# Performance work log

Hardware: AMD Instinct MI355X
Metric: run time of the kernel (lower is better)

## Reference

```python
import jax, jax.numpy as jnp
import numpy as np

B, T, A, H = 2048, 512, 32, 16


def setup_inputs() -> dict:
    key = jax.random.key(0)
    ks = jax.random.split(key, 10)
    s = 1.0 / np.sqrt(H)
    inputs = jax.random.normal(ks[0], (B, T, A), dtype=jnp.float32)
    masks = (jax.random.uniform(ks[1], (B, T)) > 0.05).astype(jnp.float32)
    h0 = jnp.zeros((1, B, H), dtype=jnp.float32)
    c0 = jnp.zeros((1, B, H), dtype=jnp.float32)
    # torch nn.LSTM params (gate order i,f,g,o) and linear heads
    w_ih = jax.random.uniform(ks[2], (4 * H, A), minval=-s, maxval=s)
    w_hh = jax.random.uniform(ks[3], (4 * H, H), minval=-s, maxval=s)
    b_ih = jax.random.uniform(ks[4], (4 * H,), minval=-s, maxval=s)
    b_hh = jax.random.uniform(ks[5], (4 * H,), minval=-s, maxval=s)
    w_actor = jax.random.uniform(ks[6], (A, H), minval=-s, maxval=s)
    b_actor = jax.random.uniform(ks[7], (A,), minval=-s, maxval=s)
    w_critic = jax.random.uniform(ks[8], (1, H), minval=-s, maxval=s)
    b_critic = jax.random.uniform(ks[9], (1,), minval=-s, maxval=s)
    return {"inputs": inputs, "masks": masks, "h0": h0, "c0": c0,
            "w_ih": w_ih, "w_hh": w_hh, "b_ih": b_ih, "b_hh": b_hh,
            "w_actor": w_actor, "b_actor": b_actor,
            "w_critic": w_critic, "b_critic": b_critic}


def reference(inputs, masks, h0, c0, w_ih, w_hh, b_ih, b_hh,
              w_actor, b_actor, w_critic, b_critic):
    # masked LSTM scan: state is zeroed where mask==0 before each step
    def step(carry, xm):
        h, c = carry                      # [B,H]
        x, m = xm                         # x:[B,A], m:[B]
        h = h * m[:, None]
        c = c * m[:, None]
        gates = x @ w_ih.T + b_ih + h @ w_hh.T + b_hh   # [B,4H]
        i, f, g, o = jnp.split(gates, 4, axis=-1)
        i = jax.nn.sigmoid(i)
        f = jax.nn.sigmoid(f)
        g = jnp.tanh(g)
        o = jax.nn.sigmoid(o)
        c2 = f * c + i * g
        h2 = o * jnp.tanh(c2)
        return (h2, c2), h2

    xs = (jnp.swapaxes(inputs, 0, 1), masks.T)          # time-major
    (hT, cT), feats = jax.lax.scan(step, (h0[0], c0[0]), xs)
    feats = jnp.swapaxes(feats, 0, 1)                   # [B,T,H]
    actor = feats @ w_actor.T + b_actor                 # [B,T,A]
    critic = feats @ w_critic.T + b_critic              # [B,T,1]
    return actor, critic, hT[None], cT[None]
```

## Files before the change

### kernel.cpp

```cpp
#include <hip/hip_runtime.h>
#include <stdint.h>

#define Bn 2048
#define Tn 512
#define An 32
#define Hn 16

typedef __attribute__((ext_vector_type(8))) short bf16x8;
typedef __attribute__((ext_vector_type(4))) float f32x4;

union FragU { bf16x8 v; uint32_t u[4]; };

static __device__ __forceinline__ uint32_t pack_hi16(float a, float b){
  return (__float_as_uint(b) & 0xFFFF0000u) | (__float_as_uint(a) >> 16);
}
static __device__ __forceinline__ void split8(const float* s, FragU& hi, FragU& lo){
#pragma unroll
  for (int d = 0; d < 4; ++d){
    float a = s[2*d], b = s[2*d+1];
    float ah = __uint_as_float(__float_as_uint(a) & 0xFFFF0000u);
    float bh = __uint_as_float(__float_as_uint(b) & 0xFFFF0000u);
    hi.u[d] = pack_hi16(a, b);
    lo.u[d] = pack_hi16(a - ah, b - bh);
  }
}
static __device__ __forceinline__ uint32_t plo(uint32_t e, uint32_t o){
  return __builtin_amdgcn_perm(o, e, 0x05040100u);
}
static __device__ __forceinline__ uint32_t phi(uint32_t e, uint32_t o){
  return __builtin_amdgcn_perm(o, e, 0x07060302u);
}
static __device__ __forceinline__ f32x4 MF(const FragU& a, const FragU& b, f32x4 c){
  return __builtin_amdgcn_mfma_f32_16x16x32_bf16(a.v, b.v, c, 0, 0, 0);
}
static __device__ __forceinline__ void packH(const float* hs, uint32_t* pk){
#pragma unroll
  for (int r = 0; r < 4; ++r){
    float hh_ = __uint_as_float(__float_as_uint(hs[r]) & 0xFFFF0000u);
    pk[r] = (__float_as_uint(hs[r] - hh_) & 0xFFFF0000u) | (__float_as_uint(hs[r]) >> 16);
  }
}
static __device__ __forceinline__ void buildBH(const uint32_t* pk, int srcA, int srcB,
                                               FragU& BHh, FragU& BHl){
  uint32_t d0 = (uint32_t)__builtin_amdgcn_ds_bpermute(srcA, (int)pk[0]);
  uint32_t d1 = (uint32_t)__builtin_amdgcn_ds_bpermute(srcA, (int)pk[1]);
  uint32_t d2 = (uint32_t)__builtin_amdgcn_ds_bpermute(srcA, (int)pk[2]);
  uint32_t d3 = (uint32_t)__builtin_amdgcn_ds_bpermute(srcA, (int)pk[3]);
  uint32_t d4 = (uint32_t)__builtin_amdgcn_ds_bpermute(srcB, (int)pk[0]);
  uint32_t d5 = (uint32_t)__builtin_amdgcn_ds_bpermute(srcB, (int)pk[1]);
  uint32_t d6 = (uint32_t)__builtin_amdgcn_ds_bpermute(srcB, (int)pk[2]);
  uint32_t d7 = (uint32_t)__builtin_amdgcn_ds_bpermute(srcB, (int)pk[3]);
  BHh.u[0] = plo(d0, d1); BHh.u[1] = plo(d2, d3);
  BHh.u[2] = plo(d4, d5); BHh.u[3] = plo(d6, d7);
  BHl.u[0] = phi(d0, d1); BHl.u[1] = phi(d2, d3);
  BHl.u[2] = phi(d4, d5); BHl.u[3] = phi(d6, d7);
}

__global__ __launch_bounds__(64, 1)
void lstm_fused(const float* __restrict__ xin,
                const float* __restrict__ masks,
                const float* __restrict__ h0,
                const float* __restrict__ c0,
                const float* __restrict__ w_ih,
                const float* __restrict__ w_hh,
                const float* __restrict__ b_ih,
                const float* __restrict__ b_hh,
                const float* __restrict__ w_act,
                const float* __restrict__ b_act,
                const float* __restrict__ w_cr,
                const float* __restrict__ b_cr,
                float* __restrict__ actor,
                float* __restrict__ critic,
                float* __restrict__ hT,
                float* __restrict__ cT)
{
  const int l = threadIdx.x;
  const int q = l >> 4;
  const int n = l & 15;
  const int b0 = blockIdx.x * 16;
  const int colbase = (q & 1) * 8;
  const bool hiQuad = (q < 2);

  const float KS = -1.44269504088896f;
  const float KG =  2.88539008177793f;

  FragU wihH0, wihL0, whh10, whh20; f32x4 bias0;
  FragU wihH1, wihL1, whh11, whh21; f32x4 bias1;
  FragU wihH2, wihL2, whh12, whh22; f32x4 bias2;
  FragU wihH3, wihL3, whh13, whh23; f32x4 bias3;
  {
    auto loadGate = [&](int g, float sc, FragU& wh, FragU& wl, FragU& a1, FragU& a2, f32x4& bg){
      float tmp[8];
#pragma unroll
      for (int j = 0; j < 8; ++j) tmp[j] = w_ih[(g*16 + n)*32 + q*8 + j] * sc;
      split8(tmp, wh, wl);
#pragma unroll
      for (int j = 0; j < 8; ++j) tmp[j] = w_hh[(g*16 + n)*16 + colbase + j] * sc;
      FragU hh, hl; split8(tmp, hh, hl);
#pragma unroll
      for (int d = 0; d < 4; ++d){
        a1.u[d] = hiQuad ? hh.u[d] : hl.u[d];
        a2.u[d] = hiQuad ? hh.u[d] : 0u;
      }
#pragma unroll
      for (int r = 0; r < 4; ++r)
        bg[r] = (b_ih[g*16 + q*4 + r] + b_hh[g*16 + q*4 + r]) * sc;
    };
    loadGate(0, KS, wihH0, wihL0, whh10, whh20, bias0);
    loadGate(1, KS, wihH1, wihL1, whh11, whh21, bias1);
    loadGate(2, KG, wihH2, wihL2, whh12, whh22, bias2);
    loadGate(3, KS, wihH3, wihL3, whh13, whh23, bias3);
  }

  FragU whA10, whA20, whA11, whA21, wcA1, wcA2;
  f32x4 biasA0, biasA1;
  const float bcr = b_cr[0];
  {
    float tmp[8];
#pragma unroll
    for (int j = 0; j < 8; ++j) tmp[j] = w_act[(0*16 + n)*16 + colbase + j];
    { FragU hh, hl; split8(tmp, hh, hl);
#pragma unroll
      for (int d = 0; d < 4; ++d){ whA10.u[d] = hiQuad ? hh.u[d] : hl.u[d]; whA20.u[d] = hiQuad ? hh.u[d] : 0u; } }
#pragma unroll
    for (int r = 0; r < 4; ++r) biasA0[r] = b_act[0*16 + q*4 + r];
#pragma unroll
    for (int j = 0; j < 8; ++j) tmp[j] = w_act[(1*16 + n)*16 + colbase + j];
    { FragU hh, hl; split8(tmp, hh, hl);
#pragma unroll
      for (int d = 0; d < 4; ++d){ whA11.u[d] = hiQuad ? hh.u[d] : hl.u[d]; whA21.u[d] = hiQuad ? hh.u[d] : 0u; } }
#pragma unroll
    for (int r = 0; r < 4; ++r) biasA1[r] = b_act[1*16 + q*4 + r];
#pragma unroll
    for (int j = 0; j < 8; ++j) tmp[j] = (n == 0) ? w_cr[colbase + j] : 0.0f;
    { FragU hh, hl; split8(tmp, hh, hl);
#pragma unroll
      for (int d = 0; d < 4; ++d){ wcA1.u[d] = hiQuad ? hh.u[d] : hl.u[d]; wcA2.u[d] = hiQuad ? hh.u[d] : 0u; } }
  }

  const int srcA = (((q & 1) * 2) * 16 + n) * 4;
  const int srcB = srcA + 64;

  float cs[4], hs[4];
#pragma unroll
  for (int r = 0; r < 4; ++r){
    hs[r] = h0[(b0 + n)*16 + q*4 + r];
    cs[r] = c0[(b0 + n)*16 + q*4 + r];
  }
  uint32_t pk[4];
  packH(hs, pk);
  FragU BHh, BHl;
  buildBH(pk, srcA, srcB, BHh, BHl);

  const f32x4 zero4 = {0.f, 0.f, 0.f, 0.f};

  const size_t xrow = (size_t)(b0 + n) * Tn * 32 + q * 8;
  float4 xA[4], xB[4];
#pragma unroll
  for (int u = 0; u < 4; ++u){
    xA[u] = *(const float4*)&xin[xrow + (size_t)u * 32];
    xB[u] = *(const float4*)&xin[xrow + (size_t)u * 32 + 4];
  }
  const size_t mrow = (size_t)(b0 + n) * Tn;
  float mCur = masks[mrow];

  for (int t0 = 0; t0 < Tn; t0 += 4){
#pragma unroll
    for (int u = 0; u < 4; ++u){
      const int t = t0 + u;
      const float m = mCur;
      {
        const int tm = (t + 1 < Tn) ? (t + 1) : t;
        mCur = masks[mrow + tm];
      }
      float cm[4];
#pragma unroll
      for (int r = 0; r < 4; ++r) cm[r] = cs[r] * m;

      FragU Xh, Xl;
      {
        float s[8] = {xA[u].x, xA[u].y, xA[u].z, xA[u].w,
                      xB[u].x, xB[u].y, xB[u].z, xB[u].w};
        split8(s, Xh, Xl);
      }
      {
        const int tn = (t + 4 < Tn) ? (t + 4) : t;
        xA[u] = *(const float4*)&xin[xrow + (size_t)tn * 32];
        xB[u] = *(const float4*)&xin[xrow + (size_t)tn * 32 + 4];
      }

      f32x4 ax0 = MF(wihH0, Xh, bias0); ax0 = MF(wihH0, Xl, ax0); ax0 = MF(wihL0, Xh, ax0);
      f32x4 ax1 = MF(wihH1, Xh, bias1); ax1 = MF(wihH1, Xl, ax1); ax1 = MF(wihL1, Xh, ax1);
      f32x4 ax2 = MF(wihH2, Xh, bias2); ax2 = MF(wihH2, Xl, ax2); ax2 = MF(wihL2, Xh, ax2);
      f32x4 ax3 = MF(wihH3, Xh, bias3); ax3 = MF(wihH3, Xl, ax3); ax3 = MF(wihL3, Xh, ax3);

      f32x4 ah0 = MF(whh10, BHh, zero4); ah0 = MF(whh20, BHl, ah0);
      f32x4 ah1 = MF(whh11, BHh, zero4); ah1 = MF(whh21, BHl, ah1);
      f32x4 ah2 = MF(whh12, BHh, zero4); ah2 = MF(whh22, BHl, ah2);
      f32x4 ah3 = MF(whh13, BHh, zero4); ah3 = MF(whh23, BHl, ah3);

      if (t){
        const int th = t - 1;
        f32x4 a0 = MF(whA10, BHh, biasA0); a0 = MF(whA20, BHl, a0);
        *(f32x4*)&actor[((size_t)(b0 + n) * Tn + th) * 32 + 0*16 + q*4] = a0;
        f32x4 a1 = MF(whA11, BHh, biasA1); a1 = MF(whA21, BHl, a1);
        *(f32x4*)&actor[((size_t)(b0 + n) * Tn + th) * 32 + 1*16 + q*4] = a1;
        f32x4 cc = MF(wcA1, BHh, zero4); cc = MF(wcA2, BHl, cc);
        if (q == 0) critic[(size_t)(b0 + n) * Tn + th] = cc[0] + bcr;
      }

#pragma unroll
      for (int r = 0; r < 4; ++r){
        float gi = ax0[r] + m * ah0[r];
        float gf = ax1[r] + m * ah1[r];
        float gg = ax2[r] + m * ah2[r];
        float go = ax3[r] + m * ah3[r];
        float iv = __builtin_amdgcn_rcpf(1.0f + __builtin_amdgcn_exp2f(gi));
        float fv = __builtin_amdgcn_rcpf(1.0f + __builtin_amdgcn_exp2f(gf));
        float gr = __builtin_amdgcn_rcpf(1.0f + __builtin_amdgcn_exp2f(gg));
        float ov = __builtin_amdgcn_rcpf(1.0f + __builtin_amdgcn_exp2f(go));
        float gv = 1.0f - 2.0f * gr;
        float c2 = fv * cm[r] + iv * gv;
        float r2 = __builtin_amdgcn_rcpf(1.0f + __builtin_amdgcn_exp2f(c2 * KG));
        float orr = ov * r2;
        float h2 = ov - 2.0f * orr;
        cs[r] = c2;
        hs[r] = h2;
      }
      packH(hs, pk);
      buildBH(pk, srcA, srcB, BHh, BHl);
    }
  }

  {
    const int th = Tn - 1;
    f32x4 a0 = MF(whA10, BHh, biasA0); a0 = MF(whA20, BHl, a0);
    *(f32x4*)&actor[((size_t)(b0 + n) * Tn + th) * 32 + 0*16 + q*4] = a0;
    f32x4 a1 = MF(whA11, BHh, biasA1); a1 = MF(whA21, BHl, a1);
    *(f32x4*)&actor[((size_t)(b0 + n) * Tn + th) * 32 + 1*16 + q*4] = a1;
    f32x4 cc = MF(wcA1, BHh, zero4); cc = MF(wcA2, BHl, cc);
    if (q == 0) critic[(size_t)(b0 + n) * Tn + th] = cc[0] + bcr;
  }
  *(float4*)&hT[(b0 + n)*16 + q*4] = make_float4(hs[0], hs[1], hs[2], hs[3]);
  *(float4*)&cT[(b0 + n)*16 + q*4] = make_float4(cs[0], cs[1], cs[2], cs[3]);
}

extern "C" void kernel_launch(void* const* d_in, const int* in_sizes, int n_in,
                              void* d_out, int out_size, void* d_ws, size_t ws_size,
                              hipStream_t stream) {
  (void)in_sizes; (void)n_in; (void)out_size; (void)d_ws; (void)ws_size;
  const float* xin   = (const float*)d_in[0];
  const float* masks = (const float*)d_in[1];
  const float* h0    = (const float*)d_in[2];
  const float* c0    = (const float*)d_in[3];
  const float* w_ih  = (const float*)d_in[4];
  const float* w_hh  = (const float*)d_in[5];
  const float* b_ih  = (const float*)d_in[6];
  const float* b_hh  = (const float*)d_in[7];
  const float* w_act = (const float*)d_in[8];
  const float* b_act = (const float*)d_in[9];
  const float* w_cr  = (const float*)d_in[10];
  const float* b_cr  = (const float*)d_in[11];

  float* out    = (float*)d_out;
  float* actor  = out;
  float* critic = out + (size_t)Bn * Tn * An;
  float* hT     = critic + (size_t)Bn * Tn;
  float* cT     = hT + (size_t)Bn * Hn;

  lstm_fused<<<Bn/16, 64, 0, stream>>>(xin, masks, h0, c0, w_ih, w_hh, b_ih, b_hh,
                                       w_act, b_act, w_cr, b_cr,
                                       actor, critic, hT, cT);
}
```

Baseline: 520.9 us.

## Use single lane-selected hidden-state fragment, vectorize mask loads, batch transcendentals

Reorganizes the split-bf16 recurrent matmul so each lane's B fragment carries either the high or low half of h, chosen by a per-quad byte-select perm. This halves the perm work and the live fragment registers, with the weight fragments rearranged to match. Mask values are now loaded four timesteps at a time as float4 instead of one scalar load per step. The gate nonlinearity is restructured so all exp2 and rcp calls are issued in batches for better ILP. The risk is a subtle change in precision-term pairing that must still cover the hi*hi, hi*lo and lo*hi products.

```diff
diff --git a/kernel.cpp b/kernel.cpp
--- a/kernel.cpp
+++ b/kernel.cpp
@@ -24,12 +24,6 @@
     lo.u[d] = pack_hi16(a - ah, b - bh);
   }
 }
-static __device__ __forceinline__ uint32_t plo(uint32_t e, uint32_t o){
-  return __builtin_amdgcn_perm(o, e, 0x05040100u);
-}
-static __device__ __forceinline__ uint32_t phi(uint32_t e, uint32_t o){
-  return __builtin_amdgcn_perm(o, e, 0x07060302u);
-}
 static __device__ __forceinline__ f32x4 MF(const FragU& a, const FragU& b, f32x4 c){
   return __builtin_amdgcn_mfma_f32_16x16x32_bf16(a.v, b.v, c, 0, 0, 0);
 }
@@ -40,8 +34,8 @@
     pk[r] = (__float_as_uint(hs[r] - hh_) & 0xFFFF0000u) | (__float_as_uint(hs[r]) >> 16);
   }
 }
-static __device__ __forceinline__ void buildBH(const uint32_t* pk, int srcA, int srcB,
-                                               FragU& BHh, FragU& BHl){
+static __device__ __forceinline__ void buildB1(const uint32_t* pk, int srcA, int srcB,
+                                               uint32_t bsel, FragU& B1){
   uint32_t d0 = (uint32_t)__builtin_amdgcn_ds_bpermute(srcA, (int)pk[0]);
   uint32_t d1 = (uint32_t)__builtin_amdgcn_ds_bpermute(srcA, (int)pk[1]);
   uint32_t d2 = (uint32_t)__builtin_amdgcn_ds_bpermute(srcA, (int)pk[2]);
@@ -50,10 +44,10 @@
   uint32_t d5 = (uint32_t)__builtin_amdgcn_ds_bpermute(srcB, (int)pk[1]);
   uint32_t d6 = (uint32_t)__builtin_amdgcn_ds_bpermute(srcB, (int)pk[2]);
   uint32_t d7 = (uint32_t)__builtin_amdgcn_ds_bpermute(srcB, (int)pk[3]);
-  BHh.u[0] = plo(d0, d1); BHh.u[1] = plo(d2, d3);
-  BHh.u[2] = plo(d4, d5); BHh.u[3] = plo(d6, d7);
-  BHl.u[0] = phi(d0, d1); BHl.u[1] = phi(d2, d3);
-  BHl.u[2] = phi(d4, d5); BHl.u[3] = phi(d6, d7);
+  B1.u[0] = __builtin_amdgcn_perm(d1, d0, bsel);
+  B1.u[1] = __builtin_amdgcn_perm(d3, d2, bsel);
+  B1.u[2] = __builtin_amdgcn_perm(d5, d4, bsel);
+  B1.u[3] = __builtin_amdgcn_perm(d7, d6, bsel);
 }
 
 __global__ __launch_bounds__(64, 1)
@@ -80,6 +74,7 @@
   const int b0 = blockIdx.x * 16;
   const int colbase = (q & 1) * 8;
   const bool hiQuad = (q < 2);
+  const uint32_t bsel = hiQuad ? 0x05040100u : 0x07060302u;
 
   const float KS = -1.44269504088896f;
   const float KG =  2.88539008177793f;
@@ -99,8 +94,8 @@
       FragU hh, hl; split8(tmp, hh, hl);
 #pragma unroll
       for (int d = 0; d < 4; ++d){
-        a1.u[d] = hiQuad ? hh.u[d] : hl.u[d];
-        a2.u[d] = hiQuad ? hh.u[d] : 0u;
+        a1.u[d] = hh.u[d];
+        a2.u[d] = hiQuad ? hl.u[d] : 0u;
       }
 #pragma unroll
       for (int r = 0; r < 4; ++r)
@@ -121,21 +116,21 @@
     for (int j = 0; j < 8; ++j) tmp[j] = w_act[(0*16 + n)*16 + colbase + j];
     { FragU hh, hl; split8(tmp, hh, hl);
 #pragma unroll
-      for (int d = 0; d < 4; ++d){ whA10.u[d] = hiQuad ? hh.u[d] : hl.u[d]; whA20.u[d] = hiQuad ? hh.u[d] : 0u; } }
+      for (int d = 0; d < 4; ++d){ whA10.u[d] = hh.u[d]; whA20.u[d] = hiQuad ? hl.u[d] : 0u; } }
 #pragma unroll
     for (int r = 0; r < 4; ++r) biasA0[r] = b_act[0*16 + q*4 + r];
 #pragma unroll
     for (int j = 0; j < 8; ++j) tmp[j] = w_act[(1*16 + n)*16 + colbase + j];
     { FragU hh, hl; split8(tmp, hh, hl);
 #pragma unroll
-      for (int d = 0; d < 4; ++d){ whA11.u[d] = hiQuad ? hh.u[d] : hl.u[d]; whA21.u[d] = hiQuad ? hh.u[d] : 0u; } }
+      for (int d = 0; d < 4; ++d){ whA11.u[d] = hh.u[d]; whA21.u[d] = hiQuad ? hl.u[d] : 0u; } }
 #pragma unroll
     for (int r = 0; r < 4; ++r) biasA1[r] = b_act[1*16 + q*4 + r];
 #pragma unroll
     for (int j = 0; j < 8; ++j) tmp[j] = (n == 0) ? w_cr[colbase + j] : 0.0f;
     { FragU hh, hl; split8(tmp, hh, hl);
 #pragma unroll
-      for (int d = 0; d < 4; ++d){ wcA1.u[d] = hiQuad ? hh.u[d] : hl.u[d]; wcA2.u[d] = hiQuad ? hh.u[d] : 0u; } }
+      for (int d = 0; d < 4; ++d){ wcA1.u[d] = hh.u[d]; wcA2.u[d] = hiQuad ? hl.u[d] : 0u; } }
   }
 
   const int srcA = (((q & 1) * 2) * 16 + n) * 4;
@@ -149,8 +144,8 @@
   }
   uint32_t pk[4];
   packH(hs, pk);
-  FragU BHh, BHl;
-  buildBH(pk, srcA, srcB, BHh, BHl);
+  FragU B1;
+  buildB1(pk, srcA, srcB, bsel, B1);
 
   const f32x4 zero4 = {0.f, 0.f, 0.f, 0.f};
 
@@ -162,17 +157,15 @@
     xB[u] = *(const float4*)&xin[xrow + (size_t)u * 32 + 4];
   }
   const size_t mrow = (size_t)(b0 + n) * Tn;
-  float mCur = masks[mrow];
+  float4 mQ = *(const float4*)&masks[mrow];
 
   for (int t0 = 0; t0 < Tn; t0 += 4){
+    const int tb = (t0 + 4 < Tn) ? (t0 + 4) : 0;
+    float4 mN = *(const float4*)&masks[mrow + tb];
 #pragma unroll
     for (int u = 0; u < 4; ++u){
       const int t = t0 + u;
-      const float m = mCur;
-      {
-        const int tm = (t + 1 < Tn) ? (t + 1) : t;
-        mCur = masks[mrow + tm];
-      }
+      const float m = (u == 0) ? mQ.x : (u == 1) ? mQ.y : (u == 2) ? mQ.z : mQ.w;
       float cm[4];
 #pragma unroll
       for (int r = 0; r < 4; ++r) cm[r] = cs[r] * m;
@@ -194,51 +187,64 @@
       f32x4 ax2 = MF(wihH2, Xh, bias2); ax2 = MF(wihH2, Xl, ax2); ax2 = MF(wihL2, Xh, ax2);
       f32x4 ax3 = MF(wihH3, Xh, bias3); ax3 = MF(wihH3, Xl, ax3); ax3 = MF(wihL3, Xh, ax3);
 
-      f32x4 ah0 = MF(whh10, BHh, zero4); ah0 = MF(whh20, BHl, ah0);
-      f32x4 ah1 = MF(whh11, BHh, zero4); ah1 = MF(whh21, BHl, ah1);
-      f32x4 ah2 = MF(whh12, BHh, zero4); ah2 = MF(whh22, BHl, ah2);
-      f32x4 ah3 = MF(whh13, BHh, zero4); ah3 = MF(whh23, BHl, ah3);
+      f32x4 ah0 = MF(whh10, B1, zero4); ah0 = MF(whh20, B1, ah0);
+      f32x4 ah1 = MF(whh11, B1, zero4); ah1 = MF(whh21, B1, ah1);
+      f32x4 ah2 = MF(whh12, B1, zero4); ah2 = MF(whh22, B1, ah2);
+      f32x4 ah3 = MF(whh13, B1, zero4); ah3 = MF(whh23, B1, ah3);
 
       if (t){
         const int th = t - 1;
-        f32x4 a0 = MF(whA10, BHh, biasA0); a0 = MF(whA20, BHl, a0);
+        f32x4 a0 = MF(whA10, B1, biasA0); a0 = MF(whA20, B1, a0);
         *(f32x4*)&actor[((size_t)(b0 + n) * Tn + th) * 32 + 0*16 + q*4] = a0;
-        f32x4 a1 = MF(whA11, BHh, biasA1); a1 = MF(whA21, BHl, a1);
+        f32x4 a1 = MF(whA11, B1, biasA1); a1 = MF(whA21, B1, a1);
         *(f32x4*)&actor[((size_t)(b0 + n) * Tn + th) * 32 + 1*16 + q*4] = a1;
-        f32x4 cc = MF(wcA1, BHh, zero4); cc = MF(wcA2, BHl, cc);
+        f32x4 cc = MF(wcA1, B1, zero4); cc = MF(wcA2, B1, cc);
         if (q == 0) critic[(size_t)(b0 + n) * Tn + th] = cc[0] + bcr;
       }
 
+      float gt[16];
 #pragma unroll
       for (int r = 0; r < 4; ++r){
-        float gi = ax0[r] + m * ah0[r];
-        float gf = ax1[r] + m * ah1[r];
-        float gg = ax2[r] + m * ah2[r];
-        float go = ax3[r] + m * ah3[r];
-        float iv = __builtin_amdgcn_rcpf(1.0f + __builtin_amdgcn_exp2f(gi));
-        float fv = __builtin_amdgcn_rcpf(1.0f + __builtin_amdgcn_exp2f(gf));
-        float gr = __builtin_amdgcn_rcpf(1.0f + __builtin_amdgcn_exp2f(gg));
-        float ov = __builtin_amdgcn_rcpf(1.0f + __builtin_amdgcn_exp2f(go));
-        float gv = 1.0f - 2.0f * gr;
-        float c2 = fv * cm[r] + iv * gv;
-        float r2 = __builtin_amdgcn_rcpf(1.0f + __builtin_amdgcn_exp2f(c2 * KG));
-        float orr = ov * r2;
-        float h2 = ov - 2.0f * orr;
-        cs[r] = c2;
-        hs[r] = h2;
+        gt[r]      = ax0[r] + m * ah0[r];
+        gt[4 + r]  = ax1[r] + m * ah1[r];
+        gt[8 + r]  = ax2[r] + m * ah2[r];
+        gt[12 + r] = ax3[r] + m * ah3[r];
+      }
+      float ex[16];
+#pragma unroll
+      for (int j = 0; j < 16; ++j) ex[j] = __builtin_amdgcn_exp2f(gt[j]);
+#pragma unroll
+      for (int j = 0; j < 16; ++j) ex[j] = __builtin_amdgcn_rcpf(1.0f + ex[j]);
+      float c2v[4];
+#pragma unroll
+      for (int r = 0; r < 4; ++r){
+        float gv = 1.0f - 2.0f * ex[8 + r];
+        c2v[r] = ex[4 + r] * cm[r] + ex[r] * gv;
+        cs[r] = c2v[r];
+      }
+      float et[4];
+#pragma unroll
+      for (int r = 0; r < 4; ++r) et[r] = __builtin_amdgcn_exp2f(c2v[r] * KG);
+#pragma unroll
+      for (int r = 0; r < 4; ++r) et[r] = __builtin_amdgcn_rcpf(1.0f + et[r]);
+#pragma unroll
+      for (int r = 0; r < 4; ++r){
+        float ov = ex[12 + r];
+        hs[r] = ov - 2.0f * (ov * et[r]);
       }
       packH(hs, pk);
-      buildBH(pk, srcA, srcB, BHh, BHl);
+      buildB1(pk, srcA, srcB, bsel, B1);
     }
+    mQ = mN;
   }
 
   {
     const int th = Tn - 1;
-    f32x4 a0 = MF(whA10, BHh, biasA0); a0 = MF(whA20, BHl, a0);
+    f32x4 a0 = MF(whA10, B1, biasA0); a0 = MF(whA20, B1, a0);
     *(f32x4*)&actor[((size_t)(b0 + n) * Tn + th) * 32 + 0*16 + q*4] = a0;
-    f32x4 a1 = MF(whA11, BHh, biasA1); a1 = MF(whA21, BHl, a1);
+    f32x4 a1 = MF(whA11, B1, biasA1); a1 = MF(whA21, B1, a1);
     *(f32x4*)&actor[((size_t)(b0 + n) * Tn + th) * 32 + 1*16 + q*4] = a1;
-    f32x4 cc = MF(wcA1, BHh, zero4); cc = MF(wcA2, BHl, cc);
+    f32x4 cc = MF(wcA1, B1, zero4); cc = MF(wcA2, B1, cc);
     if (q == 0) critic[(size_t)(b0 + n) * Tn + th] = cc[0] + bcr;
   }
   *(float4*)&hT[(b0 + n)*16 + q*4] = make_float4(hs[0], hs[1], hs[2], hs[3]);
```

Measured after the change: 535.5 us. +2.8%, slower.
